# Performance work log

Hardware: AMD Instinct MI355X
Metric: run time of the kernel (lower is better)

The kernel has to match this reference:

```python
import jax, jax.numpy as jnp
import numpy as np
import math

DIM_IN, DIM_OUT, DIM_HID = 128, 128, 512
DEPTH, HEADS, DIM_HEAD, MLP = 6, 8, 64, 2048
INNER = HEADS * DIM_HEAD  # 512


def _inorm(t, eps=1e-5):
    # torch InstanceNorm1d on ((b h), n, d): normalize over last (spatial) dim, biased var, no affine
    m = jnp.mean(t, axis=-1, keepdims=True)
    v = jnp.mean((t - m) ** 2, axis=-1, keepdims=True)
    return (t - m) * jax.lax.rsqrt(v + eps)


def _layernorm(t, g, b, eps=1e-5):
    m = jnp.mean(t, axis=-1, keepdims=True)
    v = jnp.mean((t - m) ** 2, axis=-1, keepdims=True)
    return (t - m) * jax.lax.rsqrt(v + eps) * g + b


def _pos_encoding(n, d):
    pos = jnp.arange(n, dtype=jnp.float32)[:, None]
    div = jnp.exp(jnp.arange(0, d, 2, dtype=jnp.float32) * (-math.log(10000.0) / d))
    pe = jnp.zeros((n, d), dtype=jnp.float32)
    pe = pe.at[:, 0::2].set(jnp.sin(pos * div))
    pe = pe.at[:, 1::2].set(jnp.cos(pos * div))
    return pe


def setup_inputs() -> dict:
    key = jax.random.key(0)
    ks = jax.random.split(key, 16)
    s = 0.02
    return {
        "x": jax.random.normal(ks[0], (4, 64, 4096, 2), jnp.float32),
        "W_emb": jax.random.normal(ks[1], (DIM_IN, DIM_HID), jnp.float32) * s,
        "b_emb": jnp.zeros((DIM_HID,), jnp.float32),
        "ln_g": jnp.ones((DEPTH, DIM_HID), jnp.float32),
        "ln_b": jnp.zeros((DEPTH, DIM_HID), jnp.float32),
        "Wqkv": jax.random.normal(ks[2], (DEPTH, DIM_HID, 3 * INNER), jnp.float32) * s,
        "Wout": jax.random.normal(ks[3], (DEPTH, INNER, DIM_HID), jnp.float32) * s,
        "b_out": jnp.zeros((DEPTH, DIM_HID), jnp.float32),
        "W1": jax.random.normal(ks[4], (DEPTH, DIM_HID, 2 * MLP), jnp.float32) * s,
        "b1": jnp.zeros((DEPTH, 2 * MLP), jnp.float32),
        "W2": jax.random.normal(ks[5], (DEPTH, MLP, DIM_HID), jnp.float32) * s,
        "b2": jnp.zeros((DEPTH, DIM_HID), jnp.float32),
        "Wd": jax.random.normal(ks[6], (DIM_HID, DIM_OUT), jnp.float32) * s,
        "bd": jnp.zeros((DIM_OUT,), jnp.float32),
    }


def reference(x, W_emb, b_emb, ln_g, ln_b, Wqkv, Wout, b_out, W1, b1, W2, b2, Wd, bd):
    b, t, n, c = x.shape
    h = x.transpose(0, 2, 1, 3).reshape(b, n, t * c)        # [b, n, dim_in]
    h = (h @ W_emb + b_emb) * math.sqrt(DIM_HID)
    h = h + _pos_encoding(n, DIM_HID)[None]                 # positional encoding (dropout=0)
    inv_n = 1.0 / n
    for i in range(DEPTH):
        # PreNorm(LinearAttention) + residual
        y = _layernorm(h, ln_g[i], ln_b[i])
        qkv = y @ Wqkv[i]                                   # [b, n, 3*inner]
        q, k, v = jnp.split(qkv, 3, axis=-1)
        sp = lambda z: z.reshape(b, n, HEADS, DIM_HEAD).transpose(0, 2, 1, 3)  # b h n d
        q, k, v = sp(q), sp(k), sp(v)
        k, v = _inorm(k), _inorm(v)                         # galerkin: norm K and V
        dots = jnp.einsum('bhnd,bhne->bhde', k, v)          # k^T v: O(n) attention
        o = jnp.einsum('bhnd,bhde->bhne', q, dots) * inv_n
        o = o.transpose(0, 2, 1, 3).reshape(b, n, INNER)
        h = o @ Wout[i] + b_out[i] + h
        # FeedForward (no PreNorm in galerkin branch) + residual
        f = h @ W1[i] + b1[i]
        f = jax.nn.gelu(f[..., :MLP], approximate=False) * f[..., MLP:]
        h = f @ W2[i] + b2[i] + h
    out = h @ Wd + bd                                       # [b, n, dim_out]
    return out.transpose(0, 2, 1).reshape(b, -1, 1)         # [b, dim_out*n, 1]
```

## Files before the change

kernel.cpp:

```cpp
#include <hip/hip_runtime.h>
#include <hip/hip_bf16.h>
#include <stdint.h>
#include <math.h>


typedef _Float16 f16x8 __attribute__((ext_vector_type(8)));
typedef float f32x4 __attribute__((ext_vector_type(4)));
typedef unsigned short u16x8 __attribute__((ext_vector_type(8)));
typedef unsigned short u16;

#define SEQ 4096
#define NTOK 16384
#define HID 512
#define RSCL 256.0f
#define RSCLI (1.0f/256.0f)

__device__ __forceinline__ float wred(float x) {
#pragma unroll
  for (int off = 32; off; off >>= 1) x += __shfl_xor(x, off);
  return x;
}

__device__ __forceinline__ u16 f2h(float v) {
  _Float16 h = (_Float16)v;
  return __builtin_bit_cast(u16, h);
}
__device__ __forceinline__ float h2f(u16 u) {
  return (float)__builtin_bit_cast(_Float16, u);
}

__device__ __forceinline__ void gload16(const void* g, void* l) {
  __builtin_amdgcn_global_load_lds(
      reinterpret_cast<const __attribute__((address_space(1))) int*>(
          reinterpret_cast<uintptr_t>(g)),
      reinterpret_cast<__attribute__((address_space(3))) int*>(
          reinterpret_cast<uintptr_t>(l)),
      16, 0, 0);
}

__global__ __launch_bounds__(256) void k_transpose(const float* __restrict__ src,
                                                   u16* __restrict__ dst,
                                                   int K, int N) {
  int d = blockIdx.z;
  const float* s = src + (size_t)d * K * N;
  u16* o = dst + (size_t)d * N * K;
  int k0 = blockIdx.x * 64, n0 = blockIdx.y * 64;
  __shared__ float tile[64][65];
  int t = threadIdx.x, c = t & 63, r4 = t >> 6;
#pragma unroll
  for (int i = 0; i < 16; ++i) {
    int r = i * 4 + r4;
    tile[r][c] = s[(size_t)(k0 + r) * N + n0 + c];
  }
  __syncthreads();
#pragma unroll
  for (int i = 0; i < 16; ++i) {
    int r = i * 4 + r4;
    o[(size_t)(n0 + r) * K + k0 + c] = f2h(tile[c][r]);
  }
}

__global__ __launch_bounds__(256) void k_packx(const float* __restrict__ x,
                                               u16* __restrict__ XP) {
  int idx = blockIdx.x * 256 + threadIdx.x;
  int k = idx & 127, row = idx >> 7;
  int b = row >> 12, n = row & 4095;
  int tt = k >> 1, c = k & 1;
  XP[idx] = f2h(x[(((size_t)(b * 64 + tt)) * SEQ + n) * 2 + c]);
}

__global__ __launch_bounds__(256) void k_ln(const float* __restrict__ H,
                                            const float* __restrict__ G,
                                            const float* __restrict__ B,
                                            u16* __restrict__ Y) {
  int t = threadIdx.x, lane = t & 63;
  int row = blockIdx.x * 4 + (t >> 6);
  const float4* h4 = (const float4*)(H + (size_t)row * HID);
  float4 a = h4[lane * 2], b = h4[lane * 2 + 1];
  float v[8] = {a.x, a.y, a.z, a.w, b.x, b.y, b.z, b.w};
  float s = v[0] + v[1] + v[2] + v[3] + v[4] + v[5] + v[6] + v[7];
  s = wred(s);
  float m = s * (1.0f / 512.0f);
  float q = 0.f;
#pragma unroll
  for (int i = 0; i < 8; ++i) {
    v[i] -= m;
    q += v[i] * v[i];
  }
  q = wred(q);
  float rs = rsqrtf(q * (1.0f / 512.0f) + 1e-5f);
  const float4* g4 = (const float4*)G;
  const float4* b4 = (const float4*)B;
  float4 g1 = g4[lane * 2], g2 = g4[lane * 2 + 1];
  float4 e1 = b4[lane * 2], e2 = b4[lane * 2 + 1];
  float gg[8] = {g1.x, g1.y, g1.z, g1.w, g2.x, g2.y, g2.z, g2.w};
  float ee[8] = {e1.x, e1.y, e1.z, e1.w, e2.x, e2.y, e2.z, e2.w};
  union { u16x8 v; u16 s_[8]; } uh;
#pragma unroll
  for (int i = 0; i < 8; ++i) uh.s_[i] = f2h(v[i] * rs * gg[i] + ee[i]);
  *reinterpret_cast<u16x8*>((u16*)Y + (size_t)row * HID + lane * 8) = uh.v;
}

__global__ __launch_bounds__(256) void k_dots(const u16* __restrict__ QKV,
                                              float* __restrict__ DOTSP) {
  int bh = blockIdx.y, b = bh >> 3, h = bh & 7;
  int n0 = blockIdx.x * 512;
  __shared__ alignas(16) short ks[64 * 64];
  __shared__ alignas(16) short vs[64 * 64];
  int t = threadIdx.x;
  int d0 = (t & 15) * 4, e0 = (t >> 4) * 4;
  float acc[4][4] = {};
  for (int sub = 0; sub < 8; ++sub) {
    int nb = n0 + sub * 64;
#pragma unroll
    for (int i = 0; i < 2; ++i) {
      int c = t + i * 256;
      int r = c >> 3, off = (c & 7) << 3;
      const u16* base = QKV + (size_t)(b * SEQ + nb + r) * 1536;
      gload16(base + 512 + h * 64 + off, ks + c * 8);
      gload16(base + 1024 + h * 64 + off, vs + c * 8);
    }
    asm volatile("s_waitcnt vmcnt(0)" ::: "memory");
    __syncthreads();
    for (int r = 0; r < 64; ++r) {
      short4 kk = *(const short4*)&ks[r * 64 + d0];
      short4 vv = *(const short4*)&vs[r * 64 + e0];
      float kf[4] = {h2f((u16)kk.x), h2f((u16)kk.y), h2f((u16)kk.z), h2f((u16)kk.w)};
      float vf[4] = {h2f((u16)vv.x), h2f((u16)vv.y), h2f((u16)vv.z), h2f((u16)vv.w)};
#pragma unroll
      for (int i = 0; i < 4; ++i)
#pragma unroll
        for (int j = 0; j < 4; ++j) acc[i][j] += kf[i] * vf[j];
    }
    __syncthreads();
  }
  float* dst = DOTSP + ((size_t)blockIdx.x * 32 + bh) * 4096;
#pragma unroll
  for (int i = 0; i < 4; ++i)
#pragma unroll
    for (int j = 0; j < 4; ++j) dst[(d0 + i) * 64 + e0 + j] = acc[i][j];
}

__global__ __launch_bounds__(256) void k_reddots(const float* __restrict__ P,
                                                 float* __restrict__ D) {
  int i = blockIdx.x * 256 + threadIdx.x;
  float s = 0.f;
#pragma unroll
  for (int c = 0; c < 8; ++c) s += P[(size_t)c * 131072 + i];
  D[i] = s;
}

__global__ __launch_bounds__(256) void k_ov(const u16* __restrict__ QKV,
                                            const float* __restrict__ DOTS,
                                            u16* __restrict__ O) {
  int bh = blockIdx.y, b = bh >> 3, h = bh & 7;
  int n0 = blockIdx.x * 64;
  __shared__ alignas(16) float ds[64 * 64];
  __shared__ alignas(16) short qs[64 * 64];
  int t = threadIdx.x;
  const float* dsrc = DOTS + (size_t)bh * 4096;
#pragma unroll
  for (int i = 0; i < 16; ++i) ds[t + i * 256] = dsrc[t + i * 256];
#pragma unroll
  for (int i = 0; i < 2; ++i) {
    int c = t + i * 256, r = c >> 3, off = (c & 7) << 3;
    gload16(QKV + (size_t)(b * SEQ + n0 + r) * 1536 + h * 64 + off, qs + c * 8);
  }
  asm volatile("s_waitcnt vmcnt(0)" ::: "memory");
  __syncthreads();
  int wv = t >> 6, lane = t & 63;
  for (int tok = wv; tok < 64; tok += 4) {
    float acc = 0.f;
#pragma unroll
    for (int d = 0; d < 64; d += 4) {
      short4 q4 = *(const short4*)&qs[tok * 64 + d];
      acc += h2f((u16)q4.x) * ds[(d + 0) * 64 + lane];
      acc += h2f((u16)q4.y) * ds[(d + 1) * 64 + lane];
      acc += h2f((u16)q4.z) * ds[(d + 2) * 64 + lane];
      acc += h2f((u16)q4.w) * ds[(d + 3) * 64 + lane];
    }
    O[(size_t)(b * SEQ + n0 + tok) * 512 + h * 64 + lane] = f2h(acc * (1.0f / SEQ));
  }
}

__device__ __forceinline__ void stage_t(const u16* g, int ldk, int rowBase,
                                        int k0, short* lds, int t) {
#pragma unroll
  for (int i = 0; i < 2; ++i) {
    int c = t + i * 256;
    int r = c >> 2, ko = (c & 3) << 3;
    gload16(g + (size_t)(rowBase + r) * ldk + k0 + ko, lds + c * 8);
  }
}

template <int MODE>
__global__ __launch_bounds__(256, 2) void k_gemm(
    const u16* __restrict__ A, const u16* __restrict__ B1,
    const u16* __restrict__ B2, int K,
    const float* __restrict__ bias, const float* __restrict__ Hin,
    float ascale, float* __restrict__ out32, u16* __restrict__ o16, int ldo) {
  constexpr bool GATED = (MODE == 5);
  constexpr int NTILE = GATED ? 3 : 2;
  __shared__ alignas(16) short sm[2][NTILE][128 * 32];
  const int t = threadIdx.x, lane = t & 63;
  const int wv = t >> 6, wr = wv >> 1, wc = wv & 1;
  const int r16 = lane & 15, grp = lane >> 4;
  const int mBase = blockIdx.y * 128, nBase = blockIdx.x * 128;
  const int NT = K >> 5;

  f32x4 acc[4][4] = {};
  f32x4 acc2[GATED ? 4 : 1][GATED ? 4 : 1] = {};

  auto stage_all = [&](int sb, int k0) {
    stage_t(A, K, mBase, k0, &sm[sb][0][0], t);
    stage_t(B1, K, nBase, k0, &sm[sb][1][0], t);
    if constexpr (GATED) stage_t(B2, K, nBase, k0, &sm[sb][2][0], t);
  };

  stage_all(0, 0);
  asm volatile("s_waitcnt vmcnt(0)" ::: "memory");
  __syncthreads();

  int buf = 0;
  for (int kt = 0; kt < NT; ++kt) {
    if (kt + 1 < NT) stage_all(buf ^ 1, (kt + 1) << 5);
    const int fo = grp * 8;
    f16x8 af[4], b1v[4];
#pragma unroll
    for (int f = 0; f < 4; ++f)
      af[f] = *(const f16x8*)&sm[buf][0][(wr * 64 + f * 16 + r16) * 32 + fo];
#pragma unroll
    for (int f = 0; f < 4; ++f)
      b1v[f] = *(const f16x8*)&sm[buf][1][(wc * 64 + f * 16 + r16) * 32 + fo];
#pragma unroll
    for (int i = 0; i < 4; ++i)
#pragma unroll
      for (int j = 0; j < 4; ++j)
        acc[i][j] = __builtin_amdgcn_mfma_f32_16x16x32_f16(af[i], b1v[j], acc[i][j], 0, 0, 0);
    if constexpr (GATED) {
      f16x8 b2v[4];
#pragma unroll
      for (int f = 0; f < 4; ++f)
        b2v[f] = *(const f16x8*)&sm[buf][2][(wc * 64 + f * 16 + r16) * 32 + fo];
#pragma unroll
      for (int i = 0; i < 4; ++i)
#pragma unroll
        for (int j = 0; j < 4; ++j)
          acc2[i][j] = __builtin_amdgcn_mfma_f32_16x16x32_f16(af[i], b2v[j], acc2[i][j], 0, 0, 0);
    }
    if (kt + 1 < NT) {
      asm volatile("s_waitcnt vmcnt(0)" ::: "memory");
      __syncthreads();
      buf ^= 1;
    }
  }

  if constexpr (MODE == 1) {
    const bool doNorm = (nBase >= 512);
#pragma unroll
    for (int i = 0; i < 4; ++i) {
#pragma unroll
      for (int r = 0; r < 4; ++r) {
        float s = 0.f, s2 = 0.f;
#pragma unroll
        for (int j = 0; j < 4; ++j) {
          float v = acc[i][j][r];
          s += v;
          s2 += v * v;
        }
#pragma unroll
        for (int off = 8; off; off >>= 1) {
          s += __shfl_xor(s, off);
          s2 += __shfl_xor(s2, off);
        }
        float m = s * (1.0f / 64.0f);
        float var = fmaxf(s2 * (1.0f / 64.0f) - m * m, 0.f);
        float rs = rsqrtf(var + 1e-5f);
        int row = mBase + wr * 64 + i * 16 + grp * 4 + r;
#pragma unroll
        for (int j = 0; j < 4; ++j) {
          int col = nBase + wc * 64 + j * 16 + r16;
          float v = acc[i][j][r];
          if (doNorm) v = (v - m) * rs;
          o16[(size_t)row * ldo + col] = f2h(v);
        }
      }
    }
    return;
  }

#pragma unroll
  for (int i = 0; i < 4; ++i) {
#pragma unroll
    for (int j = 0; j < 4; ++j) {
#pragma unroll
      for (int r = 0; r < 4; ++r) {
        int row = mBase + wr * 64 + i * 16 + grp * 4 + r;
        int col = nBase + wc * 64 + j * 16 + r16;
        float v = acc[i][j][r];
        if constexpr (MODE == 0) {
          v = (v + bias[col]) * 22.627416997969522f;
          int n = row & (SEQ - 1);
          int k2 = col >> 1;
          float ang = (float)n * expf((float)k2 * -0.03597789207803197f);
          v += (col & 1) ? cosf(ang) : sinf(ang);
          out32[(size_t)row * HID + col] = v;
        } else if constexpr (MODE == 2) {
          v = v * ascale + bias[col] + Hin[(size_t)row * HID + col];
          out32[(size_t)row * HID + col] = v;
          o16[(size_t)row * HID + col] = f2h(v * RSCLI);
        } else if constexpr (MODE == 7) {
          v = v * RSCL + bias[col];
          out32[(size_t)(row >> 12) * (128 * 4096) + (size_t)col * SEQ + (row & 4095)] = v;
        } else {
          float a = v * RSCL + bias[col];
          float c2 = acc2[i][j][r] * RSCL + bias[2048 + col];
          float gl = 0.5f * a * (1.0f + erff(a * 0.7071067811865475f));
          o16[(size_t)row * ldo + col] = f2h(gl * c2 * RSCLI);
        }
      }
    }
  }
}

extern "C" void kernel_launch(void* const* d_in, const int* in_sizes, int n_in,
                              void* d_out, int out_size, void* d_ws, size_t ws_size,
                              hipStream_t stream) {
  const float* x    = (const float*)d_in[0];
  const float* Wemb = (const float*)d_in[1];
  const float* bemb = (const float*)d_in[2];
  const float* lng  = (const float*)d_in[3];
  const float* lnb  = (const float*)d_in[4];
  const float* Wqkv = (const float*)d_in[5];
  const float* Wout = (const float*)d_in[6];
  const float* bout = (const float*)d_in[7];
  const float* W1   = (const float*)d_in[8];
  const float* b1   = (const float*)d_in[9];
  const float* W2   = (const float*)d_in[10];
  const float* b2   = (const float*)d_in[11];
  const float* Wd   = (const float*)d_in[12];
  const float* bd   = (const float*)d_in[13];

  char* p = (char*)d_ws;
  auto alloc = [&](size_t bytes) {
    char* r = p;
    p += (bytes + 255) & ~(size_t)255;
    return r;
  };
  u16* WembT = (u16*)alloc((size_t)512 * 128 * 2);
  u16* WqkvT = (u16*)alloc((size_t)6 * 1536 * 512 * 2);
  u16* WoutT = (u16*)alloc((size_t)6 * 512 * 512 * 2);
  u16* W1T   = (u16*)alloc((size_t)6 * 4096 * 512 * 2);
  u16* W2T   = (u16*)alloc((size_t)6 * 512 * 2048 * 2);
  u16* WdT   = (u16*)alloc((size_t)128 * 512 * 2);
  float* H   = (float*)alloc((size_t)NTOK * 512 * 4);
  u16* HB    = (u16*)alloc((size_t)NTOK * 512 * 2);
  float* DOTSP = (float*)alloc((size_t)8 * 32 * 4096 * 4);
  float* DOTS  = (float*)alloc((size_t)32 * 4096 * 4);
  char* U = alloc((size_t)64 * 1024 * 1024);
  const size_t MI = 1024 * 1024;
  u16* XP  = (u16*)U;
  u16* Y   = (u16*)U;
  u16* QKV = (u16*)(U + 16 * MI);
  u16* O   = (u16*)U;
  u16* F   = (u16*)U;

  k_transpose<<<dim3(2, 8, 1),  256, 0, stream>>>(Wemb, WembT, 128, 512);
  k_transpose<<<dim3(8, 24, 6), 256, 0, stream>>>(Wqkv, WqkvT, 512, 1536);
  k_transpose<<<dim3(8, 8, 6),  256, 0, stream>>>(Wout, WoutT, 512, 512);
  k_transpose<<<dim3(8, 64, 6), 256, 0, stream>>>(W1, W1T, 512, 4096);
  k_transpose<<<dim3(32, 8, 6), 256, 0, stream>>>(W2, W2T, 2048, 512);
  k_transpose<<<dim3(8, 2, 1),  256, 0, stream>>>(Wd, WdT, 512, 128);

  k_packx<<<8192, 256, 0, stream>>>(x, XP);
  k_gemm<0><<<dim3(4, 128), 256, 0, stream>>>(XP, WembT, nullptr, 128, bemb,
      nullptr, 1.f, H, nullptr, 0);

  for (int i = 0; i < 6; ++i) {
    k_ln<<<4096, 256, 0, stream>>>(H, lng + i * 512, lnb + i * 512, Y);
    k_gemm<1><<<dim3(12, 128), 256, 0, stream>>>(Y,
        WqkvT + (size_t)i * 1536 * 512, nullptr, 512,
        nullptr, nullptr, 1.f, nullptr, QKV, 1536);
    k_dots<<<dim3(8, 32), 256, 0, stream>>>(QKV, DOTSP);
    k_reddots<<<512, 256, 0, stream>>>(DOTSP, DOTS);
    k_ov<<<dim3(64, 32), 256, 0, stream>>>(QKV, DOTS, O);
    k_gemm<2><<<dim3(4, 128), 256, 0, stream>>>(O,
        WoutT + (size_t)i * 512 * 512, nullptr, 512,
        bout + i * 512, H, 1.f, H, HB, 512);
    k_gemm<5><<<dim3(16, 128), 256, 0, stream>>>(HB,
        W1T + (size_t)i * 4096 * 512,
        W1T + (size_t)i * 4096 * 512 + (size_t)2048 * 512, 512,
        b1 + i * 4096, nullptr, 1.f, nullptr, F, 2048);
    k_gemm<2><<<dim3(4, 128), 256, 0, stream>>>(F,
        W2T + (size_t)i * 512 * 2048, nullptr, 2048,
        b2 + i * 512, H, RSCL, H, HB, 512);
  }
  k_gemm<7><<<dim3(1, 128), 256, 0, stream>>>(HB, WdT, nullptr, 512, bd,
      nullptr, 1.f, (float*)d_out, nullptr, 0);
}
```

Baseline: 1.911 ms.

## Add large-tile swizzled GEMM kernels for QKV and gated FFN with fast GELU

Replaces the generic 128x128 GEMM for the QKV projection with a 512-thread 256x256-tile kernel using XOR-swizzled LDS, split K-phase staging and MFMA priority boosting. The gated FFN GEMM gets a similar 512-thread 128x256 kernel that interleaves loads of the two weight halves with compute. The exact erf GELU is swapped for a tanh-based approximation using __expf. The aim is more reuse per LDS load, fewer bank conflicts and a cheaper epilogue, at the cost of higher register/LDS pressure and a small numerical deviation from exact GELU.

```diff
diff --git a/kernel.cpp b/kernel.cpp
--- a/kernel.cpp
+++ b/kernel.cpp
@@ -27,6 +27,13 @@
 }
 __device__ __forceinline__ float h2f(u16 u) {
   return (float)__builtin_bit_cast(_Float16, u);
+}
+
+__device__ __forceinline__ float fgelu(float a) {
+  float t = 0.7978845608f * a * (1.0f + 0.044715f * a * a);
+  float e = __expf(2.0f * t);
+  float th = 1.0f - 2.0f / (e + 1.0f);
+  return 0.5f * a * (1.0f + th);
 }
 
 __device__ __forceinline__ void gload16(const void* g, void* l) {
@@ -183,6 +190,219 @@
   }
 }
 
+__device__ __forceinline__ void stP(const u16* g, int ldk, int rowBase, int k0,
+                                    short* lds, int t, int i) {
+  int c = t + i * 512;
+  int r = c >> 3, s = (c & 7) ^ (r & 7);
+  gload16(g + (size_t)(rowBase + r) * ldk + k0 + s * 8, lds + c * 8);
+}
+
+__global__ __launch_bounds__(512, 2) void k_gemmP(
+    const u16* __restrict__ A, int lda, const u16* __restrict__ BT, int K,
+    u16* __restrict__ o16, int ldo) {
+  __shared__ alignas(16) short sm[2][2][16384];
+  const int t = threadIdx.x, lane = t & 63;
+  const int w = t >> 6, wr = w >> 2, wcn = w & 3;
+  const int r16 = lane & 15, grp = lane >> 4;
+  const int mBase = blockIdx.y * 256, nBase = blockIdx.x * 256;
+  const int NT = K >> 6;
+
+  f32x4 acc[8][4] = {};
+
+#pragma unroll
+  for (int i = 0; i < 4; ++i) stP(A, lda, mBase, 0, &sm[0][0][0], t, i);
+#pragma unroll
+  for (int i = 0; i < 4; ++i) stP(BT, K, nBase, 0, &sm[0][1][0], t, i);
+  __syncthreads();
+
+  int buf = 0;
+  for (int kt = 0; kt < NT; ++kt) {
+    int k0n = (kt + 1) << 6;
+    if (kt + 1 < NT) {
+#pragma unroll
+      for (int i = 0; i < 4; ++i) stP(A, lda, mBase, k0n, &sm[buf ^ 1][0][0], t, i);
+    }
+    {
+      f16x8 af[8], bf[4];
+#pragma unroll
+      for (int i = 0; i < 8; ++i) {
+        int row = wr * 128 + i * 16 + r16;
+        af[i] = *(const f16x8*)&sm[buf][0][row * 64 + ((grp) ^ (row & 7)) * 8];
+      }
+#pragma unroll
+      for (int j = 0; j < 4; ++j) {
+        int row = wcn * 64 + j * 16 + r16;
+        bf[j] = *(const f16x8*)&sm[buf][1][row * 64 + ((grp) ^ (row & 7)) * 8];
+      }
+      __builtin_amdgcn_s_barrier();
+      asm volatile("s_waitcnt lgkmcnt(0)" ::: "memory");
+      __builtin_amdgcn_sched_barrier(0);
+      __builtin_amdgcn_s_setprio(1);
+#pragma unroll
+      for (int i = 0; i < 8; ++i)
+#pragma unroll
+        for (int j = 0; j < 4; ++j)
+          acc[i][j] = __builtin_amdgcn_mfma_f32_16x16x32_f16(af[i], bf[j], acc[i][j], 0, 0, 0);
+      __builtin_amdgcn_s_setprio(0);
+    }
+    if (kt + 1 < NT) {
+#pragma unroll
+      for (int i = 0; i < 4; ++i) stP(BT, K, nBase, k0n, &sm[buf ^ 1][1][0], t, i);
+    }
+    {
+      f16x8 af[8], bf[4];
+#pragma unroll
+      for (int i = 0; i < 8; ++i) {
+        int row = wr * 128 + i * 16 + r16;
+        af[i] = *(const f16x8*)&sm[buf][0][row * 64 + ((4 + grp) ^ (row & 7)) * 8];
+      }
+#pragma unroll
+      for (int j = 0; j < 4; ++j) {
+        int row = wcn * 64 + j * 16 + r16;
+        bf[j] = *(const f16x8*)&sm[buf][1][row * 64 + ((4 + grp) ^ (row & 7)) * 8];
+      }
+      __builtin_amdgcn_s_barrier();
+      asm volatile("s_waitcnt lgkmcnt(0)" ::: "memory");
+      __builtin_amdgcn_sched_barrier(0);
+      __builtin_amdgcn_s_setprio(1);
+#pragma unroll
+      for (int i = 0; i < 8; ++i)
+#pragma unroll
+        for (int j = 0; j < 4; ++j)
+          acc[i][j] = __builtin_amdgcn_mfma_f32_16x16x32_f16(af[i], bf[j], acc[i][j], 0, 0, 0);
+      __builtin_amdgcn_s_setprio(0);
+    }
+    asm volatile("s_waitcnt vmcnt(0)" ::: "memory");
+    __builtin_amdgcn_s_barrier();
+    buf ^= 1;
+  }
+
+  const bool doNorm = (nBase + wcn * 64) >= 512;
+#pragma unroll
+  for (int i = 0; i < 8; ++i) {
+#pragma unroll
+    for (int r = 0; r < 4; ++r) {
+      float s = 0.f, s2 = 0.f;
+#pragma unroll
+      for (int j = 0; j < 4; ++j) {
+        float v = acc[i][j][r];
+        s += v;
+        s2 += v * v;
+      }
+#pragma unroll
+      for (int off = 8; off; off >>= 1) {
+        s += __shfl_xor(s, off);
+        s2 += __shfl_xor(s2, off);
+      }
+      float m = s * (1.0f / 64.0f);
+      float var = fmaxf(s2 * (1.0f / 64.0f) - m * m, 0.f);
+      float rs = rsqrtf(var + 1e-5f);
+      int row = mBase + wr * 128 + i * 16 + grp * 4 + r;
+#pragma unroll
+      for (int j = 0; j < 4; ++j) {
+        int col = nBase + wcn * 64 + j * 16 + r16;
+        float v = acc[i][j][r];
+        if (doNorm) v = (v - m) * rs;
+        o16[(size_t)row * ldo + col] = f2h(v);
+      }
+    }
+  }
+}
+
+__device__ __forceinline__ void stG(const u16* g, int ldk, int rowBase, int k0,
+                                    short* lds, int t, int i) {
+  int c = t + i * 512;
+  int pr = c >> 3, s8 = (c & 7) ^ (pr & 7);
+  int r = pr * 2 + (s8 >> 2);
+  gload16(g + (size_t)(rowBase + r) * ldk + k0 + (s8 & 3) * 8, lds + c * 8);
+}
+
+#define IDXG(row) (((row) >> 1) * 64 + (((((row) & 1) << 2) | grp) ^ (((row) >> 1) & 7)) * 8)
+
+__global__ __launch_bounds__(512, 2) void k_gemmG(
+    const u16* __restrict__ A, int lda,
+    const u16* __restrict__ B1, const u16* __restrict__ B2, int K,
+    const float* __restrict__ bias, u16* __restrict__ o16, int ldo) {
+  __shared__ alignas(16) short sm[2][20480];
+  const int t = threadIdx.x, lane = t & 63;
+  const int w = t >> 6, wr = w >> 2, wcn = w & 3;
+  const int r16 = lane & 15, grp = lane >> 4;
+  const int mBase = blockIdx.y * 128, nBase = blockIdx.x * 256;
+  const int NT = K >> 5;
+
+  f32x4 acc[4][4] = {};
+  f32x4 acc2[4][4] = {};
+
+  stG(A, lda, mBase, 0, &sm[0][0], t, 0);
+#pragma unroll
+  for (int i = 0; i < 2; ++i) stG(B1, K, nBase, 0, &sm[0][4096], t, i);
+#pragma unroll
+  for (int i = 0; i < 2; ++i) stG(B2, K, nBase, 0, &sm[0][12288], t, i);
+  __syncthreads();
+
+  int buf = 0;
+  for (int kt = 0; kt < NT; ++kt) {
+    int k0n = (kt + 1) << 5;
+    f16x8 af[4], bv[4];
+    if (kt + 1 < NT) {
+      stG(A, lda, mBase, k0n, &sm[buf ^ 1][0], t, 0);
+#pragma unroll
+      for (int i = 0; i < 2; ++i) stG(B1, K, nBase, k0n, &sm[buf ^ 1][4096], t, i);
+    }
+#pragma unroll
+    for (int i = 0; i < 4; ++i)
+      af[i] = *(const f16x8*)&sm[buf][IDXG(wr * 64 + i * 16 + r16)];
+#pragma unroll
+    for (int j = 0; j < 4; ++j)
+      bv[j] = *(const f16x8*)&sm[buf][4096 + IDXG(wcn * 64 + j * 16 + r16)];
+    __builtin_amdgcn_s_barrier();
+    asm volatile("s_waitcnt lgkmcnt(0)" ::: "memory");
+    __builtin_amdgcn_sched_barrier(0);
+    __builtin_amdgcn_s_setprio(1);
+#pragma unroll
+    for (int i = 0; i < 4; ++i)
+#pragma unroll
+      for (int j = 0; j < 4; ++j)
+        acc[i][j] = __builtin_amdgcn_mfma_f32_16x16x32_f16(af[i], bv[j], acc[i][j], 0, 0, 0);
+    __builtin_amdgcn_s_setprio(0);
+    if (kt + 1 < NT) {
+#pragma unroll
+      for (int i = 0; i < 2; ++i) stG(B2, K, nBase, k0n, &sm[buf ^ 1][12288], t, i);
+    }
+#pragma unroll
+    for (int j = 0; j < 4; ++j)
+      bv[j] = *(const f16x8*)&sm[buf][12288 + IDXG(wcn * 64 + j * 16 + r16)];
+    __builtin_amdgcn_s_barrier();
+    asm volatile("s_waitcnt lgkmcnt(0)" ::: "memory");
+    __builtin_amdgcn_sched_barrier(0);
+    __builtin_amdgcn_s_setprio(1);
+#pragma unroll
+    for (int i = 0; i < 4; ++i)
+#pragma unroll
+      for (int j = 0; j < 4; ++j)
+        acc2[i][j] = __builtin_amdgcn_mfma_f32_16x16x32_f16(af[i], bv[j], acc2[i][j], 0, 0, 0);
+    __builtin_amdgcn_s_setprio(0);
+    asm volatile("s_waitcnt vmcnt(0)" ::: "memory");
+    __builtin_amdgcn_s_barrier();
+    buf ^= 1;
+  }
+
+#pragma unroll
+  for (int i = 0; i < 4; ++i) {
+#pragma unroll
+    for (int j = 0; j < 4; ++j) {
+#pragma unroll
+      for (int r = 0; r < 4; ++r) {
+        int row = mBase + wr * 64 + i * 16 + grp * 4 + r;
+        int col = nBase + wcn * 64 + j * 16 + r16;
+        float a = acc[i][j][r] * RSCL + bias[col];
+        float c2 = acc2[i][j][r] * RSCL + bias[2048 + col];
+        o16[(size_t)row * ldo + col] = f2h(fgelu(a) * c2 * RSCLI);
+      }
+    }
+  }
+}
+
 __device__ __forceinline__ void stage_t(const u16* g, int ldk, int rowBase,
                                         int k0, short* lds, int t) {
 #pragma unroll
@@ -195,13 +415,10 @@
 
 template <int MODE>
 __global__ __launch_bounds__(256, 2) void k_gemm(
-    const u16* __restrict__ A, const u16* __restrict__ B1,
-    const u16* __restrict__ B2, int K,
+    const u16* __restrict__ A, const u16* __restrict__ B1, int K,
     const float* __restrict__ bias, const float* __restrict__ Hin,
     float ascale, float* __restrict__ out32, u16* __restrict__ o16, int ldo) {
-  constexpr bool GATED = (MODE == 5);
-  constexpr int NTILE = GATED ? 3 : 2;
-  __shared__ alignas(16) short sm[2][NTILE][128 * 32];
+  __shared__ alignas(16) short sm[2][2][128 * 32];
   const int t = threadIdx.x, lane = t & 63;
   const int wv = t >> 6, wr = wv >> 1, wc = wv & 1;
   const int r16 = lane & 15, grp = lane >> 4;
@@ -209,21 +426,18 @@
   const int NT = K >> 5;
 
   f32x4 acc[4][4] = {};
-  f32x4 acc2[GATED ? 4 : 1][GATED ? 4 : 1] = {};
-
-  auto stage_all = [&](int sb, int k0) {
-    stage_t(A, K, mBase, k0, &sm[sb][0][0], t);
-    stage_t(B1, K, nBase, k0, &sm[sb][1][0], t);
-    if constexpr (GATED) stage_t(B2, K, nBase, k0, &sm[sb][2][0], t);
-  };
-
-  stage_all(0, 0);
+
+  stage_t(A, K, mBase, 0, &sm[0][0][0], t);
+  stage_t(B1, K, nBase, 0, &sm[0][1][0], t);
   asm volatile("s_waitcnt vmcnt(0)" ::: "memory");
   __syncthreads();
 
   int buf = 0;
   for (int kt = 0; kt < NT; ++kt) {
-    if (kt + 1 < NT) stage_all(buf ^ 1, (kt + 1) << 5);
+    if (kt + 1 < NT) {
+      stage_t(A, K, mBase, (kt + 1) << 5, &sm[buf ^ 1][0][0], t);
+      stage_t(B1, K, nBase, (kt + 1) << 5, &sm[buf ^ 1][1][0], t);
+    }
     const int fo = grp * 8;
     f16x8 af[4], b1v[4];
 #pragma unroll
@@ -237,56 +451,11 @@
 #pragma unroll
       for (int j = 0; j < 4; ++j)
         acc[i][j] = __builtin_amdgcn_mfma_f32_16x16x32_f16(af[i], b1v[j], acc[i][j], 0, 0, 0);
-    if constexpr (GATED) {
-      f16x8 b2v[4];
-#pragma unroll
-      for (int f = 0; f < 4; ++f)
-        b2v[f] = *(const f16x8*)&sm[buf][2][(wc * 64 + f * 16 + r16) * 32 + fo];
-#pragma unroll
-      for (int i = 0; i < 4; ++i)
-#pragma unroll
-        for (int j = 0; j < 4; ++j)
-          acc2[i][j] = __builtin_amdgcn_mfma_f32_16x16x32_f16(af[i], b2v[j], acc2[i][j], 0, 0, 0);
-    }
     if (kt + 1 < NT) {
       asm volatile("s_waitcnt vmcnt(0)" ::: "memory");
       __syncthreads();
       buf ^= 1;
     }
-  }
-
-  if constexpr (MODE == 1) {
-    const bool doNorm = (nBase >= 512);
-#pragma unroll
-    for (int i = 0; i < 4; ++i) {
-#pragma unroll
-      for (int r = 0; r < 4; ++r) {
-        float s = 0.f, s2 = 0.f;
-#pragma unroll
-        for (int j = 0; j < 4; ++j) {
-          float v = acc[i][j][r];
-          s += v;
-          s2 += v * v;
-        }
-#pragma unroll
-        for (int off = 8; off; off >>= 1) {
-          s += __shfl_xor(s, off);
-          s2 += __shfl_xor(s2, off);
-        }
-        float m = s * (1.0f / 64.0f);
-        float var = fmaxf(s2 * (1.0f / 64.0f) - m * m, 0.f);
-        float rs = rsqrtf(var + 1e-5f);
-        int row = mBase + wr * 64 + i * 16 + grp * 4 + r;
-#pragma unroll
-        for (int j = 0; j < 4; ++j) {
-          int col = nBase + wc * 64 + j * 16 + r16;
-          float v = acc[i][j][r];
-          if (doNorm) v = (v - m) * rs;
-          o16[(size_t)row * ldo + col] = f2h(v);
-        }
-      }
-    }
-    return;
   }
 
 #pragma unroll
@@ -309,14 +478,9 @@
           v = v * ascale + bias[col] + Hin[(size_t)row * HID + col];
           out32[(size_t)row * HID + col] = v;
           o16[(size_t)row * HID + col] = f2h(v * RSCLI);
-        } else if constexpr (MODE == 7) {
+        } else {
           v = v * RSCL + bias[col];
           out32[(size_t)(row >> 12) * (128 * 4096) + (size_t)col * SEQ + (row & 4095)] = v;
-        } else {
-          float a = v * RSCL + bias[col];
-          float c2 = acc2[i][j][r] * RSCL + bias[2048 + col];
-          float gl = 0.5f * a * (1.0f + erff(a * 0.7071067811865475f));
-          o16[(size_t)row * ldo + col] = f2h(gl * c2 * RSCLI);
         }
       }
     }
@@ -373,28 +537,25 @@
   k_transpose<<<dim3(8, 2, 1),  256, 0, stream>>>(Wd, WdT, 512, 128);
 
   k_packx<<<8192, 256, 0, stream>>>(x, XP);
-  k_gemm<0><<<dim3(4, 128), 256, 0, stream>>>(XP, WembT, nullptr, 128, bemb,
+  k_gemm<0><<<dim3(4, 128), 256, 0, stream>>>(XP, WembT, 128, bemb,
       nullptr, 1.f, H, nullptr, 0);
 
   for (int i = 0; i < 6; ++i) {
     k_ln<<<4096, 256, 0, stream>>>(H, lng + i * 512, lnb + i * 512, Y);
-    k_gemm<1><<<dim3(12, 128), 256, 0, stream>>>(Y,
-        WqkvT + (size_t)i * 1536 * 512, nullptr, 512,
-        nullptr, nullptr, 1.f, nullptr, QKV, 1536);
+    k_gemmP<<<dim3(6, 64), 512, 0, stream>>>(Y, 512,
+        WqkvT + (size_t)i * 1536 * 512, 512, QKV, 1536);
     k_dots<<<dim3(8, 32), 256, 0, stream>>>(QKV, DOTSP);
     k_reddots<<<512, 256, 0, stream>>>(DOTSP, DOTS);
     k_ov<<<dim3(64, 32), 256, 0, stream>>>(QKV, DOTS, O);
     k_gemm<2><<<dim3(4, 128), 256, 0, stream>>>(O,
-        WoutT + (size_t)i * 512 * 512, nullptr, 512,
-        bout + i * 512, H, 1.f, H, HB, 512);
-    k_gemm<5><<<dim3(16, 128), 256, 0, stream>>>(HB,
+        WoutT + (size_t)i * 512 * 512, 512, bout + i * 512, H, 1.f, H, HB, 512);
+    k_gemmG<<<dim3(8, 128), 512, 0, stream>>>(HB, 512,
         W1T + (size_t)i * 4096 * 512,
         W1T + (size_t)i * 4096 * 512 + (size_t)2048 * 512, 512,
-        b1 + i * 4096, nullptr, 1.f, nullptr, F, 2048);
+        b1 + i * 4096, F, 2048);
     k_gemm<2><<<dim3(4, 128), 256, 0, stream>>>(F,
-        W2T + (size_t)i * 512 * 2048, nullptr, 2048,
-        b2 + i * 512, H, RSCL, H, HB, 512);
-  }
-  k_gemm<7><<<dim3(1, 128), 256, 0, stream>>>(HB, WdT, nullptr, 512, bd,
+        W2T + (size_t)i * 512 * 2048, 2048, b2 + i * 512, H, RSCL, H, HB, 512);
+  }
+  k_gemm<7><<<dim3(1, 128), 256, 0, stream>>>(HB, WdT, 512, bd,
       nullptr, 1.f, (float*)d_out, nullptr, 0);
 }
```

Result: no change. 1.931 ms (+1.1%).
